# Performance work log

Measured on AMD Instinct MI355X. Metric: run time of the kernel, lower is better.

Reference implementation:

```python
import jax, jax.numpy as jnp
import numpy as np
from jax import lax

B, T, S = 64, 4096, 64


def setup_inputs() -> dict:
    key = jax.random.key(0)
    k1, k2, k3 = jax.random.split(key, 3)
    transition_potentials = jax.random.normal(k1, (S, S), dtype=jnp.float32)
    emission_potentials = jax.random.normal(k2, (B, T, S), dtype=jnp.float32)
    seq_lens = jax.random.randint(k3, (B,), 1, T + 1)
    return {
        "transition_potentials": transition_potentials,
        "emission_potentials": emission_potentials,
        "seq_lens": seq_lens,
    }


def reference(transition_potentials, emission_potentials, seq_lens):
    # potential_normalization='none', potential_scale=1.0 -> normalize is identity.
    # HMM forward algorithm: alpha[t] = logsumexp_i(alpha[t-1,i] + A[i,j]) + emis[t]
    alpha0 = emission_potentials[:, 0, :]  # [B,S]

    def step(alpha_prev, emis_t):
        # alpha_prev: [B,S]; emis_t: [B,S]; transition: [S,S]
        alpha_t = jax.nn.logsumexp(
            alpha_prev[:, :, None] + transition_potentials[None, :, :], axis=1
        ) + emis_t
        return alpha_t, alpha_t

    emis_rest = jnp.moveaxis(emission_potentials[:, 1:, :], 1, 0)  # [T-1,B,S]
    _, alphas = lax.scan(step, alpha0, emis_rest)  # [T-1,B,S]
    alpha = jnp.concatenate([alpha0[None], alphas], axis=0)  # [T,B,S]
    alpha = jnp.moveaxis(alpha, 0, 1)  # [B,T,S]
    log_Z = jax.nn.logsumexp(alpha[:, -1, :], axis=-1)  # [B]
    return alpha, log_Z
```

## Files before the change

### kernel.cpp

```cpp
#include <hip/hip_runtime.h>
#include <hip/hip_bf16.h>


#define BB 64
#define TT 4096
#define SS 64
#define C_CH 64
#define LL 64
#define WARM 24

typedef __attribute__((ext_vector_type(4))) short bh4;
typedef __attribute__((ext_vector_type(4))) float f32x4;

#define LOG2E 1.44269504088896340736f
#define LN2F  0.69314718055994530942f

__device__ __forceinline__ float fexp2(float x) {
#if __has_builtin(__builtin_amdgcn_exp2f)
    return __builtin_amdgcn_exp2f(x);
#else
    return exp2f(x);
#endif
}
__device__ __forceinline__ float flog2(float x) {
#if __has_builtin(__builtin_amdgcn_logf)
    return __builtin_amdgcn_logf(x);
#else
    return log2f(x);
#endif
}
__device__ __forceinline__ float bpermf(int idx, float v) {
    return __uint_as_float((unsigned)__builtin_amdgcn_ds_bpermute(idx, (int)__float_as_uint(v)));
}
__device__ __forceinline__ int pack_bf16(float x, float y) {
    __hip_bfloat162 h = __float22bfloat162_rn(make_float2(x, y));
    int r; __builtin_memcpy(&r, &h, 4); return r;
}
union PB2 { int i[2]; bh4 v; };

__device__ __forceinline__ f32x4 mfma16(bh4 a, bh4 b, f32x4 c) {
#if __has_builtin(__builtin_amdgcn_mfma_f32_16x16x16bf16_1k)
    return __builtin_amdgcn_mfma_f32_16x16x16bf16_1k(a, b, c, 0, 0, 0);
#else
    asm("v_mfma_f32_16x16x16_bf16 %0, %1, %2, %0" : "+v"(c) : "v"(a), "v"(b));
    return c;
#endif
}

__device__ __forceinline__ float do_step(f32x4 (&al2)[4], const f32x4 (&er)[4],
                                         const bh4 (&Af)[4][4],
                                         float M2, int idxM) {
    bh4 Bf[4];
    #pragma unroll
    for (int kb = 0; kb < 4; ++kb) {
        PB2 pb;
        pb.i[0] = pack_bf16(fexp2(al2[kb].x - M2), fexp2(al2[kb].y - M2));
        pb.i[1] = pack_bf16(fexp2(al2[kb].z - M2), fexp2(al2[kb].w - M2));
        Bf[kb] = pb.v;
    }

    float M2n = 0.f;
    #pragma unroll
    for (int jt = 0; jt < 4; ++jt) {
        f32x4 d = {0.f, 0.f, 0.f, 0.f};
        #pragma unroll
        for (int kb = 0; kb < 4; ++kb)
            d = mfma16(Af[jt][kb], Bf[kb], d);
        al2[jt].x = fmaf(er[jt].x, LOG2E, M2) + flog2(d.x);
        al2[jt].y = fmaf(er[jt].y, LOG2E, M2) + flog2(d.y);
        al2[jt].z = fmaf(er[jt].z, LOG2E, M2) + flog2(d.z);
        al2[jt].w = fmaf(er[jt].w, LOG2E, M2) + flog2(d.w);
        if (jt == 0) M2n = bpermf(idxM, al2[0].x);
    }
    return M2n;
}

__device__ __forceinline__ void load_row(f32x4 (&dst)[4],
                                         const float* __restrict__ eb,
                                         int t, int off) {
    const float* p = eb + (t & (TT - 1)) * SS + off;
    #pragma unroll
    for (int jt = 0; jt < 4; ++jt)
        dst[jt] = *(const f32x4*)(p + 16 * jt);
}

__global__ __launch_bounds__(64)
__attribute__((amdgpu_waves_per_eu(1, 1)))
void hmm_phaseA(const float* __restrict__ trans,
                const float* __restrict__ emis,
                float* __restrict__ out,
                float* __restrict__ ws_warm,
                float* __restrict__ ws_bound) {
    const int lane = threadIdx.x;
    const int n = lane & 15, q = lane >> 4;
    const int w = blockIdx.x;
    const int b = w >> 2, cg = w & 3;
    const int c = 16 * cg + n;
    const bool is_c0 = (c == 0);
    const int off = 4 * q;

    bh4 Af[4][4];
    #pragma unroll
    for (int jt = 0; jt < 4; ++jt)
        #pragma unroll
        for (int kb = 0; kb < 4; ++kb) {
            float v0 = __expf(trans[(16 * kb + 4 * q + 0) * SS + 16 * jt + n]);
            float v1 = __expf(trans[(16 * kb + 4 * q + 1) * SS + 16 * jt + n]);
            float v2 = __expf(trans[(16 * kb + 4 * q + 2) * SS + 16 * jt + n]);
            float v3 = __expf(trans[(16 * kb + 4 * q + 3) * SS + 16 * jt + n]);
            PB2 pb;
            pb.i[0] = pack_bf16(v0, v1);
            pb.i[1] = pack_bf16(v2, v3);
            Af[jt][kb] = pb.v;
        }

    const int idxM = n << 2;

    const float* eb = emis + (size_t)b * TT * SS;
    float*       ob = out  + (size_t)b * TT * SS;

    const int t0 = LL * c - (WARM + 1);

    f32x4 al2[4], e0[4], ebuf[4][4];
    load_row(al2, eb, t0, off);
    #pragma unroll
    for (int jt = 0; jt < 4; ++jt) al2[jt] = al2[jt] * LOG2E;
    load_row(e0, eb, 0, off);
    #pragma unroll
    for (int k = 0; k < 4; ++k) load_row(ebuf[k], eb, t0 + 1 + k, off);

    float M2 = bpermf(idxM, al2[0].x);

    #pragma unroll 1
    for (int g = 0; g < 6; ++g) {
        #pragma unroll
        for (int k = 0; k < 4; ++k) {
            int s = 4 * g + k + 1;
            f32x4 er[4];
            #pragma unroll
            for (int jt = 0; jt < 4; ++jt) er[jt] = ebuf[k][jt];
            load_row(ebuf[k], eb, t0 + s + 4, off);
            M2 = do_step(al2, er, Af, M2, idxM);
        }
    }
    if (lane < 16)
        ws_warm[b * C_CH + 16 * cg + lane] = al2[0].x * LN2F;

    #pragma unroll 1
    for (int g = 0; g < 16; ++g) {
        #pragma unroll
        for (int k = 0; k < 4; ++k) {
            int s = 25 + 4 * g + k;
            f32x4 er[4];
            #pragma unroll
            for (int jt = 0; jt < 4; ++jt) er[jt] = ebuf[k][jt];
            load_row(ebuf[k], eb, t0 + s + 4, off);
            M2 = do_step(al2, er, Af, M2, idxM);
            if (k == 0 && g == 0) {
                if (is_c0) {
                    #pragma unroll
                    for (int jt = 0; jt < 4; ++jt) al2[jt] = e0[jt] * LOG2E;
                }
                if (cg == 0)
                    M2 = bpermf(idxM, al2[0].x);
            }
            float* p = ob + (t0 + s) * SS + off;
            #pragma unroll
            for (int jt = 0; jt < 4; ++jt)
                *(f32x4*)(p + 16 * jt) = al2[jt] * LN2F;
        }
    }
    if (lane < 16)
        ws_bound[b * C_CH + 16 * cg + lane] = al2[0].x * LN2F;
}

__global__ __launch_bounds__(256)
void hmm_phaseC(float* __restrict__ out,
                const float* __restrict__ ws_warm,
                const float* __restrict__ ws_bound) {
    const int b = blockIdx.x, c = blockIdx.y, tid = threadIdx.x;
    __shared__ float sdelta;

    if (tid < 64) {
        float d = 0.f;
        if (tid > 0 && tid < C_CH)
            d = ws_bound[b * C_CH + tid - 1] - ws_warm[b * C_CH + tid];
        #pragma unroll
        for (int off = 1; off < C_CH; off <<= 1) {
            float v = __shfl_up(d, off, 64);
            if (tid >= off) d += v;
        }
        float dc = __shfl(d, c, 64);
        if (tid == 0) sdelta = dc;
    }
    __syncthreads();
    const float delta = sdelta;

    float4* p4 = (float4*)(out + (size_t)b * TT * SS + (size_t)c * LL * SS);
    float4 last;
    #pragma unroll
    for (int i = 0; i < 4; ++i) {
        int idx = tid + 256 * i;
        float4 v = p4[idx];
        v.x += delta; v.y += delta; v.z += delta; v.w += delta;
        p4[idx] = v;
        last = v;
    }

    if (c == C_CH - 1 && tid >= 240) {
        float mx = fmaxf(fmaxf(last.x, last.y), fmaxf(last.z, last.w));
        #pragma unroll
        for (int off = 8; off >= 1; off >>= 1)
            mx = fmaxf(mx, __shfl_xor(mx, off, 64));
        float sv = __expf(last.x - mx) + __expf(last.y - mx)
                 + __expf(last.z - mx) + __expf(last.w - mx);
        #pragma unroll
        for (int off = 8; off >= 1; off >>= 1)
            sv += __shfl_xor(sv, off, 64);
        if (tid == 240)
            out[(size_t)BB * TT * SS + b] = mx + __logf(sv);
    }
}

extern "C" void kernel_launch(void* const* d_in, const int* in_sizes, int n_in,
                              void* d_out, int out_size, void* d_ws, size_t ws_size,
                              hipStream_t stream) {
    const float* trans = (const float*)d_in[0];
    const float* emis  = (const float*)d_in[1];
    float* out = (float*)d_out;

    float* ws_warm  = (float*)d_ws;
    float* ws_bound = ws_warm + BB * C_CH;

    hmm_phaseA<<<dim3(BB * 4), dim3(64), 0, stream>>>(trans, emis, out,
                                                      ws_warm, ws_bound);
    hmm_phaseC<<<dim3(BB, C_CH), dim3(256), 0, stream>>>(out, ws_warm, ws_bound);
}
```

Measured before the change: 168.5 us.

## Split sequence into 128 chunks of 32 steps with deeper emission prefetch

Doubles the number of time chunks per batch (128 chunks of 32 steps), which halves the serial recurrence per wave and doubles the phase-A grid to 512 waves. The emission prefetch depth goes from 4 to 8 rows, and the MFMA accumulation is split into two independent chains to shorten the dependency latency. The phase-C prefix scan now runs over 128 chunk offsets through shared memory with barriers. In exchange, the fixed 24-step warmup becomes a larger share of the total work, and more registers are used for the prefetch buffer.

New measurement: 155.1 us. -8.0%, faster.

```diff
diff --git a/kernel.cpp b/kernel.cpp
--- a/kernel.cpp
+++ b/kernel.cpp
@@ -5,9 +5,10 @@
 #define BB 64
 #define TT 4096
 #define SS 64
-#define C_CH 64
-#define LL 64
+#define C_CH 128
+#define LL 32
 #define WARM 24
+#define PF 8
 
 typedef __attribute__((ext_vector_type(4))) short bh4;
 typedef __attribute__((ext_vector_type(4))) float f32x4;
@@ -62,10 +63,13 @@
     float M2n = 0.f;
     #pragma unroll
     for (int jt = 0; jt < 4; ++jt) {
-        f32x4 d = {0.f, 0.f, 0.f, 0.f};
-        #pragma unroll
-        for (int kb = 0; kb < 4; ++kb)
-            d = mfma16(Af[jt][kb], Bf[kb], d);
+        f32x4 d0 = {0.f, 0.f, 0.f, 0.f};
+        f32x4 d1 = {0.f, 0.f, 0.f, 0.f};
+        d0 = mfma16(Af[jt][0], Bf[0], d0);
+        d1 = mfma16(Af[jt][1], Bf[1], d1);
+        d0 = mfma16(Af[jt][2], Bf[2], d0);
+        d1 = mfma16(Af[jt][3], Bf[3], d1);
+        f32x4 d = d0 + d1;
         al2[jt].x = fmaf(er[jt].x, LOG2E, M2) + flog2(d.x);
         al2[jt].y = fmaf(er[jt].y, LOG2E, M2) + flog2(d.y);
         al2[jt].z = fmaf(er[jt].z, LOG2E, M2) + flog2(d.z);
@@ -94,7 +98,7 @@
     const int lane = threadIdx.x;
     const int n = lane & 15, q = lane >> 4;
     const int w = blockIdx.x;
-    const int b = w >> 2, cg = w & 3;
+    const int b = w >> 3, cg = w & 7;
     const int c = 16 * cg + n;
     const bool is_c0 = (c == 0);
     const int off = 4 * q;
@@ -121,25 +125,25 @@
 
     const int t0 = LL * c - (WARM + 1);
 
-    f32x4 al2[4], e0[4], ebuf[4][4];
+    f32x4 al2[4], e0[4], ebuf[PF][4];
     load_row(al2, eb, t0, off);
     #pragma unroll
     for (int jt = 0; jt < 4; ++jt) al2[jt] = al2[jt] * LOG2E;
     load_row(e0, eb, 0, off);
     #pragma unroll
-    for (int k = 0; k < 4; ++k) load_row(ebuf[k], eb, t0 + 1 + k, off);
+    for (int k = 0; k < PF; ++k) load_row(ebuf[k], eb, t0 + 1 + k, off);
 
     float M2 = bpermf(idxM, al2[0].x);
 
     #pragma unroll 1
-    for (int g = 0; g < 6; ++g) {
-        #pragma unroll
-        for (int k = 0; k < 4; ++k) {
-            int s = 4 * g + k + 1;
+    for (int g = 0; g < 3; ++g) {
+        #pragma unroll
+        for (int k = 0; k < PF; ++k) {
+            int s = PF * g + k + 1;
             f32x4 er[4];
             #pragma unroll
             for (int jt = 0; jt < 4; ++jt) er[jt] = ebuf[k][jt];
-            load_row(ebuf[k], eb, t0 + s + 4, off);
+            load_row(ebuf[k], eb, t0 + s + PF, off);
             M2 = do_step(al2, er, Af, M2, idxM);
         }
     }
@@ -147,14 +151,14 @@
         ws_warm[b * C_CH + 16 * cg + lane] = al2[0].x * LN2F;
 
     #pragma unroll 1
-    for (int g = 0; g < 16; ++g) {
-        #pragma unroll
-        for (int k = 0; k < 4; ++k) {
-            int s = 25 + 4 * g + k;
+    for (int g = 0; g < 4; ++g) {
+        #pragma unroll
+        for (int k = 0; k < PF; ++k) {
+            int s = WARM + 1 + PF * g + k;
             f32x4 er[4];
             #pragma unroll
             for (int jt = 0; jt < 4; ++jt) er[jt] = ebuf[k][jt];
-            load_row(ebuf[k], eb, t0 + s + 4, off);
+            load_row(ebuf[k], eb, t0 + s + PF, off);
             M2 = do_step(al2, er, Af, M2, idxM);
             if (k == 0 && g == 0) {
                 if (is_c0) {
@@ -179,27 +183,29 @@
                 const float* __restrict__ ws_warm,
                 const float* __restrict__ ws_bound) {
     const int b = blockIdx.x, c = blockIdx.y, tid = threadIdx.x;
-    __shared__ float sdelta;
-
-    if (tid < 64) {
+    __shared__ float sd[C_CH];
+
+    if (tid < C_CH) {
         float d = 0.f;
-        if (tid > 0 && tid < C_CH)
+        if (tid > 0)
             d = ws_bound[b * C_CH + tid - 1] - ws_warm[b * C_CH + tid];
-        #pragma unroll
-        for (int off = 1; off < C_CH; off <<= 1) {
-            float v = __shfl_up(d, off, 64);
-            if (tid >= off) d += v;
-        }
-        float dc = __shfl(d, c, 64);
-        if (tid == 0) sdelta = dc;
+        sd[tid] = d;
     }
     __syncthreads();
-    const float delta = sdelta;
+    #pragma unroll
+    for (int off = 1; off < C_CH; off <<= 1) {
+        float v = 0.f;
+        if (tid >= off && tid < C_CH) v = sd[tid - off];
+        __syncthreads();
+        if (tid >= off && tid < C_CH) sd[tid] += v;
+        __syncthreads();
+    }
+    const float delta = sd[c];
 
     float4* p4 = (float4*)(out + (size_t)b * TT * SS + (size_t)c * LL * SS);
     float4 last;
     #pragma unroll
-    for (int i = 0; i < 4; ++i) {
+    for (int i = 0; i < 2; ++i) {
         int idx = tid + 256 * i;
         float4 v = p4[idx];
         v.x += delta; v.y += delta; v.z += delta; v.w += delta;
@@ -232,7 +238,7 @@
     float* ws_warm  = (float*)d_ws;
     float* ws_bound = ws_warm + BB * C_CH;
 
-    hmm_phaseA<<<dim3(BB * 4), dim3(64), 0, stream>>>(trans, emis, out,
+    hmm_phaseA<<<dim3(BB * 8), dim3(64), 0, stream>>>(trans, emis, out,
                                                       ws_warm, ws_bound);
     hmm_phaseC<<<dim3(BB, C_CH), dim3(256), 0, stream>>>(out, ws_warm, ws_bound);
 }
```
